# Performance work log

Hardware: AMD Instinct MI355X
Metric: run time of the kernel (lower is better)

## Reference

```python
import jax, jax.numpy as jnp
import numpy as np

N_NODES = 50000
N_EDGES = 800000
D_IN = 128
D_HID = 128


def setup_inputs() -> dict:
    key = jax.random.key(0)
    ks = jax.random.split(key, 9)
    x = jax.random.normal(ks[0], (N_NODES, D_IN), dtype=jnp.float32)
    edge_index = jax.random.randint(ks[1], (2, N_EDGES), 0, N_NODES, dtype=jnp.int64)
    s = 1.0 / np.sqrt(D_IN)
    # SAGEConv params: lin_l acts on mean-aggregated neighbors (has bias),
    # lin_r acts on the root/self features (no bias). Stored as [in, out].
    Wl1 = jax.random.uniform(ks[2], (D_IN, D_HID), jnp.float32, -s, s)
    Wr1 = jax.random.uniform(ks[3], (D_IN, D_HID), jnp.float32, -s, s)
    b1 = jax.random.uniform(ks[4], (D_HID,), jnp.float32, -s, s)
    Wl2 = jax.random.uniform(ks[5], (D_HID, D_HID), jnp.float32, -s, s)
    Wr2 = jax.random.uniform(ks[6], (D_HID, D_HID), jnp.float32, -s, s)
    b2 = jax.random.uniform(ks[7], (D_HID,), jnp.float32, -s, s)
    return {"x": x, "edge_index": edge_index, "Wl1": Wl1, "Wr1": Wr1,
            "b1": b1, "Wl2": Wl2, "Wr2": Wr2, "b2": b2}


def _sage_conv(h, src, dst, n_nodes, Wl, Wr, b):
    # gather neighbor features, mean-aggregate at targets (PyG mean aggr)
    msg = h[src]  # [E, d]
    summed = jax.ops.segment_sum(msg, dst, num_segments=n_nodes)  # [N, d]
    cnt = jax.ops.segment_sum(jnp.ones((src.shape[0], 1), h.dtype), dst,
                              num_segments=n_nodes)  # [N, 1]
    agg = summed / jnp.maximum(cnt, 1.0)  # isolated nodes -> 0, matches scatter-mean
    return agg @ Wl + b + h @ Wr


def reference(x, edge_index, Wl1, Wr1, b1, Wl2, Wr2, b2):
    src = edge_index[0]  # source nodes j (messages flow j -> i)
    dst = edge_index[1]  # target nodes i
    n = x.shape[0]
    h = _sage_conv(x, src, dst, n, Wl1, Wr1, b1)
    h = jax.nn.relu(h)  # dropout is identity in eval mode
    out = _sage_conv(h, src, dst, n, Wl2, Wr2, b2)
    return out
```

## Files before the change

### kernel.cpp

```cpp
#include <hip/hip_runtime.h>
#include <hip/hip_bf16.h>

#define DD 128
#define BSH 8
#define CHUNK 4096
#define MM_STREAMS 1024

typedef __attribute__((ext_vector_type(8))) short short8v;
typedef __attribute__((ext_vector_type(4))) float f32x4;

static __device__ __forceinline__ ushort f2bf(float f) {
    __hip_bfloat16 b = __float2bfloat16(f);
    return *reinterpret_cast<ushort*>(&b);
}


__global__ __launch_bounds__(256) void k_prep(const int* __restrict__ ei,
                                              int* __restrict__ hist, int E, int NB, int nblk,
                                              const float* __restrict__ x,
                                              ushort* __restrict__ xbf, int n4, int castBlocks,
                                              const float* __restrict__ Wl1,
                                              const float* __restrict__ Wr1,
                                              ushort* __restrict__ Wt1,
                                              const float* __restrict__ Wl2,
                                              const float* __restrict__ Wr2,
                                              ushort* __restrict__ Wt2) {
    __shared__ int lh[256];
    int t = threadIdx.x;
    int b = blockIdx.x;

    if (b < nblk) {
        lh[t] = 0;
        __syncthreads();
        int e0 = b * CHUNK;
        int e1 = min(e0 + CHUNK, E);
        for (int e = e0 + t; e < e1; e += 256)
            atomicAdd(&lh[ei[E + e] >> BSH], 1);
        __syncthreads();
        if (t < NB) hist[b * NB + t] = lh[t];
        return;
    }
    b -= nblk;
    if (b < castBlocks) {
        int i = b * 256 + t;
        if (i < n4) {
            float4 v = reinterpret_cast<const float4*>(x)[i];
            ushort4 o;
            o.x = f2bf(v.x); o.y = f2bf(v.y); o.z = f2bf(v.z); o.w = f2bf(v.w);
            reinterpret_cast<ushort4*>(xbf)[i] = o;
        }
        return;
    }
    b -= castBlocks;
    {
        const float* Wl = (b < 128) ? Wl1 : Wl2;
        const float* Wr = (b < 128) ? Wr1 : Wr2;
        ushort* Wt = (b < 128) ? Wt1 : Wt2;
        int idx = (b & 127) * 256 + t;
        int nn = idx >> 8, k = idx & 255;
        float v = (k < 128) ? Wl[k * 128 + nn] : Wr[(k - 128) * 128 + nn];
        Wt[nn * 256 + k] = f2bf(v);
    }
}

__global__ __launch_bounds__(1024) void k_hscan(int* __restrict__ hist,
                                                int* __restrict__ bbase,
                                                int nblk, int NB, int E) {
    __shared__ int part[4][256];
    __shared__ int s[256];
    int t = threadIdx.x;
    int b = t & 255, g = t >> 8;
    int q = (nblk + 3) >> 2;
    int lo = g * q, hi = min(lo + q, nblk);
    int sum = 0;
    if (b < NB)
        for (int blk = lo; blk < hi; ++blk) sum += hist[blk * NB + b];
    part[g][b] = sum;
    __syncthreads();
    if (g == 0) s[b] = part[0][b] + part[1][b] + part[2][b] + part[3][b];
    __syncthreads();
    for (int off = 1; off < 256; off <<= 1) {
        int v = 0;
        if (g == 0 && b >= off) v = s[b - off];
        __syncthreads();
        if (g == 0) s[b] += v;
        __syncthreads();
    }
    int base = (b == 0) ? 0 : s[b - 1];
    if (g == 0 && b < NB) bbase[b] = base;
    if (t == 0) bbase[NB] = E;
    int run = base;
    for (int gg = 0; gg < g; ++gg) run += part[gg][b];
    if (b < NB)
        for (int blk = lo; blk < hi; ++blk) {
            int tmp = hist[blk * NB + b];
            hist[blk * NB + b] = run;
            run += tmp;
        }
}

__global__ __launch_bounds__(256) void k_scatter(const int* __restrict__ ei,
                                                 const int* __restrict__ hist,
                                                 uint* __restrict__ pairs, int E, int NB) {
    __shared__ int lofs[256];
    __shared__ int lh[256];
    int t = threadIdx.x;
    int blk = blockIdx.x;
    lh[t] = 0;
    if (t < NB) lofs[t] = hist[blk * NB + t];
    __syncthreads();
    int e0 = blk * CHUNK, e1 = min(e0 + CHUNK, E);
    for (int e = e0 + t; e < e1; e += 256) {
        int sN = ei[e];
        int d = ei[E + e];
        int b = d >> BSH;
        int lp = atomicAdd(&lh[b], 1);
        pairs[lofs[b] + lp] = ((uint)(d & 255) << 16) | (uint)sN;
    }
}

__global__ __launch_bounds__(256) void k_csr(const uint* __restrict__ pairs,
                                             const int* __restrict__ bbase,
                                             int* __restrict__ rowptr,
                                             ushort* __restrict__ eidx,
                                             int n, int E, int NB) {
    __shared__ int lc[256];
    __shared__ int cur[256];
    int t = threadIdx.x;
    int b = blockIdx.x;
    int node0 = b << BSH;
    lc[t] = 0;
    __syncthreads();
    int r0 = bbase[b], r1 = bbase[b + 1];
    for (int i = r0 + t; i < r1; i += 256)
        atomicAdd(&lc[pairs[i] >> 16], 1);
    __syncthreads();
    int c0 = lc[t];
#pragma unroll
    for (int off = 1; off < 256; off <<= 1) {
        int u = (t >= off) ? lc[t - off] : 0;
        __syncthreads();
        lc[t] += u;
        __syncthreads();
    }
    int rp = r0 + lc[t] - c0;
    int node = node0 + t;
    if (node < n) rowptr[node] = rp;
    if (b == NB - 1 && t == 0) rowptr[n] = E;
    cur[t] = rp;
    __syncthreads();
    for (int i = r0 + t; i < r1; i += 256) {
        uint pr = pairs[i];
        int p = atomicAdd(&cur[pr >> 16], 1);
        eidx[p] = (ushort)(pr & 0xFFFFu);
    }
}


#define ACC8(v)                                    \
    acc[0] += __uint_as_float((v).x << 16);        \
    acc[1] += __uint_as_float((v).x & 0xffff0000u);\
    acc[2] += __uint_as_float((v).y << 16);        \
    acc[3] += __uint_as_float((v).y & 0xffff0000u);\
    acc[4] += __uint_as_float((v).z << 16);        \
    acc[5] += __uint_as_float((v).z & 0xffff0000u);\
    acc[6] += __uint_as_float((v).w << 16);        \
    acc[7] += __uint_as_float((v).w & 0xffff0000u);

__global__ __launch_bounds__(256) void k_aggb(const ushort* __restrict__ hin,
                                              const int* __restrict__ rowptr,
                                              const ushort* __restrict__ eidx,
                                              ushort* __restrict__ aggout, int n) {
    int wave = (int)((blockIdx.x * (unsigned)blockDim.x + threadIdx.x) >> 6);
    int lane = threadIdx.x & 63;
    int grp = lane >> 4;
    int c16 = lane & 15;
    int node = wave * 4 + grp;
    if (node >= n) return;

    int beg = rowptr[node], end = rowptr[node + 1];
    const uint4* base = reinterpret_cast<const uint4*>(hin);

    float acc[8];
#pragma unroll
    for (int i = 0; i < 8; ++i) acc[i] = 0.f;

    for (int e = beg; e < end; e += 4) {
        int m = end - e;
        int i0 = eidx[e];
        int i1 = eidx[e + (m > 1 ? 1 : 0)];
        int i2 = eidx[e + (m > 2 ? 2 : 0)];
        int i3 = eidx[e + (m > 3 ? 3 : 0)];
        uint4 v0 = base[(size_t)i0 * 16 + c16];
        uint4 v1 = base[(size_t)i1 * 16 + c16];
        uint4 v2 = base[(size_t)i2 * 16 + c16];
        uint4 v3 = base[(size_t)i3 * 16 + c16];
        ACC8(v0);
        if (m > 1) { ACC8(v1); }
        if (m > 2) { ACC8(v2); }
        if (m > 3) { ACC8(v3); }
    }

    float inv = 1.0f / fmaxf((float)(end - beg), 1.0f);
    uint4 o;
    o.x = ((uint)f2bf(acc[1] * inv) << 16) | (uint)f2bf(acc[0] * inv);
    o.y = ((uint)f2bf(acc[3] * inv) << 16) | (uint)f2bf(acc[2] * inv);
    o.z = ((uint)f2bf(acc[5] * inv) << 16) | (uint)f2bf(acc[4] * inv);
    o.w = ((uint)f2bf(acc[7] * inv) << 16) | (uint)f2bf(acc[6] * inv);
    reinterpret_cast<uint4*>(aggout)[(size_t)node * 16 + c16] = o;
}


__global__ __launch_bounds__(256, 8) void k_mm(const ushort* __restrict__ Alow,
                                               const ushort* __restrict__ Ahigh,
                                               const ushort* __restrict__ Wt,
                                               const float* __restrict__ bias,
                                               void* __restrict__ outp,
                                               int n, int ntiles, int relu, int outBf16) {
    int t = threadIdx.x;
    int wv = t >> 6;
    int l = t & 63;
    int lr = l & 15;
    int lk = l >> 4;
    int gw = blockIdx.x * 4 + wv;
    int nt = gw & 7;
    int stream = gw >> 3;

    short8v bf[8];
    const ushort* wbase = Wt + (size_t)(nt * 16 + lr) * 256 + lk * 8;
#pragma unroll
    for (int ks = 0; ks < 8; ++ks)
        bf[ks] = *reinterpret_cast<const short8v*>(wbase + ks * 32);

    int col = nt * 16 + lr;
    float bv = bias[col];

    for (int tile = stream; tile < ntiles; tile += MM_STREAMS) {
        int m0 = tile * 16;
        int arow = m0 + lr;
        if (arow >= n) arow = n - 1;
        const ushort* alo = Alow + (size_t)arow * DD + lk * 8;
        const ushort* ahi = Ahigh + (size_t)arow * DD + lk * 8;

        f32x4 acc = (f32x4){0.f, 0.f, 0.f, 0.f};
#pragma unroll
        for (int ks = 0; ks < 4; ++ks) {
            short8v af = *reinterpret_cast<const short8v*>(alo + ks * 32);
            acc = __builtin_amdgcn_mfma_f32_16x16x32_bf16(af, bf[ks], acc, 0, 0, 0);
        }
#pragma unroll
        for (int ks = 0; ks < 4; ++ks) {
            short8v af = *reinterpret_cast<const short8v*>(ahi + ks * 32);
            acc = __builtin_amdgcn_mfma_f32_16x16x32_bf16(af, bf[ks + 4], acc, 0, 0, 0);
        }

        int row0 = m0 + lk * 4;
#pragma unroll
        for (int r = 0; r < 4; ++r) {
            int row = row0 + r;
            if (row < n) {
                float v = acc[r] + bv;
                if (relu) v = fmaxf(v, 0.f);
                if (outBf16) {
                    reinterpret_cast<ushort*>(outp)[(size_t)row * DD + col] = f2bf(v);
                } else {
                    reinterpret_cast<float*>(outp)[(size_t)row * DD + col] = v;
                }
            }
        }
    }
}


extern "C" void kernel_launch(void* const* d_in, const int* in_sizes, int n_in,
                              void* d_out, int out_size, void* d_ws, size_t ws_size,
                              hipStream_t stream) {
    const float* x   = (const float*)d_in[0];
    const int*   ei  = (const int*)d_in[1];
    const float* Wl1 = (const float*)d_in[2];
    const float* Wr1 = (const float*)d_in[3];
    const float* b1  = (const float*)d_in[4];
    const float* Wl2 = (const float*)d_in[5];
    const float* Wr2 = (const float*)d_in[6];
    const float* b2  = (const float*)d_in[7];
    float* out = (float*)d_out;

    int n = in_sizes[0] / DD;
    int E = in_sizes[1] / 2;

    int NB   = (n + 255) >> 8;
    int nblk = (E + CHUNK - 1) / CHUNK;

    char* ws = (char*)d_ws;
    size_t off = 0;
    auto take = [&](size_t bytes) -> void* {
        void* p = ws + off;
        off = (off + bytes + 255) & ~(size_t)255;
        return p;
    };
    int* rowptr    = (int*)take(((size_t)n + 1) * 4);
    int* hist      = (int*)take((size_t)nblk * NB * 4);
    int* bbase     = (int*)take(((size_t)NB + 1) * 4);
    ushort* eidx   = (ushort*)take((size_t)E * 2 + 16);
    uint* pairs    = (uint*)take((size_t)E * 4);
    ushort* xbf    = (ushort*)take((size_t)n * DD * 2);
    ushort* hbf    = (ushort*)take((size_t)n * DD * 2);
    ushort* aggbf  = (ushort*)take((size_t)n * DD * 2);
    ushort* Wt1    = (ushort*)take((size_t)DD * 256 * 2);
    ushort* Wt2    = (ushort*)take((size_t)DD * 256 * 2);

    int ntiles = (n + 15) / 16;
    int n4 = n * DD / 4;
    int castBlocks = (n4 + 255) / 256;
    int prepBlocks = nblk + castBlocks + 256;

    k_prep<<<prepBlocks, 256, 0, stream>>>(ei, hist, E, NB, nblk,
                                           x, xbf, n4, castBlocks,
                                           Wl1, Wr1, Wt1, Wl2, Wr2, Wt2);
    k_hscan<<<1, 1024, 0, stream>>>(hist, bbase, nblk, NB, E);
    k_scatter<<<nblk, 256, 0, stream>>>(ei, hist, pairs, E, NB);
    k_csr<<<NB, 256, 0, stream>>>(pairs, bbase, rowptr, eidx, n, E, NB);

    int aggBlocks = (n + 15) / 16;
    int mmBlocks  = MM_STREAMS * 8 / 4;

    k_aggb<<<aggBlocks, 256, 0, stream>>>(xbf, rowptr, eidx, aggbf, n);
    k_mm<<<mmBlocks, 256, 0, stream>>>(aggbf, xbf, Wt1, b1, hbf, n, ntiles, 1, 1);
    k_aggb<<<aggBlocks, 256, 0, stream>>>(hbf, rowptr, eidx, aggbf, n);
    k_mm<<<mmBlocks, 256, 0, stream>>>(aggbf, hbf, Wt2, b2, out, n, ntiles, 0, 0);
}
```

Before: 182.5 us.

## Stage A tiles in swizzled LDS and share across all column waves

The matmul kernel is restructured so each 512-thread block loads a 32-row strip of the concatenated [agg|h] inputs into XOR-swizzled shared memory once. Its eight waves each handle one 16-column output slice from that shared tile. Before, eight separate waves re-read the same A rows from global memory in a persistent stream loop. The cost is reloading the weight fragments per block instead of per persistent wave, plus an LDS barrier, across about 1563 blocks.

Measured after the change: 159.9 us. -12.4%, faster.

```diff
diff --git a/kernel.cpp b/kernel.cpp
--- a/kernel.cpp
+++ b/kernel.cpp
@@ -4,7 +4,6 @@
 #define DD 128
 #define BSH 8
 #define CHUNK 4096
-#define MM_STREAMS 1024
 
 typedef __attribute__((ext_vector_type(8))) short short8v;
 typedef __attribute__((ext_vector_type(4))) float f32x4;
@@ -211,55 +210,62 @@
 }
 
 
-__global__ __launch_bounds__(256, 8) void k_mm(const ushort* __restrict__ Alow,
+__global__ __launch_bounds__(512, 8) void k_mm(const ushort* __restrict__ Alow,
                                                const ushort* __restrict__ Ahigh,
                                                const ushort* __restrict__ Wt,
                                                const float* __restrict__ bias,
                                                void* __restrict__ outp,
-                                               int n, int ntiles, int relu, int outBf16) {
-    int t = threadIdx.x;
+                                               int n, int relu, int outBf16) {
+    __shared__ ushort sA[32][256];
+
+    int t = threadIdx.x;
+    int row0 = blockIdx.x * 32;
+
+#pragma unroll
+    for (int i = t; i < 1024; i += 512) {
+        int r = i >> 5, c = i & 31;
+        int row = row0 + r;
+        if (row >= n) row = n - 1;
+        const ushort* src = (c < 16) ? (Alow + (size_t)row * DD + c * 8)
+                                     : (Ahigh + (size_t)row * DD + (c - 16) * 8);
+        uint4 v = *reinterpret_cast<const uint4*>(src);
+        int cs = (c & 16) | ((c ^ r) & 15);
+        *reinterpret_cast<uint4*>(&sA[r][cs * 8]) = v;
+    }
+    __syncthreads();
+
     int wv = t >> 6;
-    int l = t & 63;
-    int lr = l & 15;
-    int lk = l >> 4;
-    int gw = blockIdx.x * 4 + wv;
-    int nt = gw & 7;
-    int stream = gw >> 3;
+    int lane = t & 63;
+    int lr = lane & 15;
+    int lk = lane >> 4;
 
     short8v bf[8];
-    const ushort* wbase = Wt + (size_t)(nt * 16 + lr) * 256 + lk * 8;
+    const ushort* wbase = Wt + (size_t)(wv * 16 + lr) * 256 + lk * 8;
 #pragma unroll
     for (int ks = 0; ks < 8; ++ks)
         bf[ks] = *reinterpret_cast<const short8v*>(wbase + ks * 32);
 
-    int col = nt * 16 + lr;
+    int col = wv * 16 + lr;
     float bv = bias[col];
 
-    for (int tile = stream; tile < ntiles; tile += MM_STREAMS) {
-        int m0 = tile * 16;
-        int arow = m0 + lr;
-        if (arow >= n) arow = n - 1;
-        const ushort* alo = Alow + (size_t)arow * DD + lk * 8;
-        const ushort* ahi = Ahigh + (size_t)arow * DD + lk * 8;
-
+#pragma unroll
+    for (int sub = 0; sub < 2; ++sub) {
+        int m0 = sub * 16;
+        int r = m0 + lr;
         f32x4 acc = (f32x4){0.f, 0.f, 0.f, 0.f};
 #pragma unroll
-        for (int ks = 0; ks < 4; ++ks) {
-            short8v af = *reinterpret_cast<const short8v*>(alo + ks * 32);
+        for (int ks = 0; ks < 8; ++ks) {
+            int cc = ks * 4 + lk;
+            int cs = (cc & 16) | ((cc ^ r) & 15);
+            short8v af = *reinterpret_cast<const short8v*>(&sA[r][cs * 8]);
             acc = __builtin_amdgcn_mfma_f32_16x16x32_bf16(af, bf[ks], acc, 0, 0, 0);
         }
-#pragma unroll
-        for (int ks = 0; ks < 4; ++ks) {
-            short8v af = *reinterpret_cast<const short8v*>(ahi + ks * 32);
-            acc = __builtin_amdgcn_mfma_f32_16x16x32_bf16(af, bf[ks + 4], acc, 0, 0, 0);
-        }
-
-        int row0 = m0 + lk * 4;
-#pragma unroll
-        for (int r = 0; r < 4; ++r) {
-            int row = row0 + r;
+        int rowb = row0 + m0 + lk * 4;
+#pragma unroll
+        for (int q = 0; q < 4; ++q) {
+            int row = rowb + q;
             if (row < n) {
-                float v = acc[r] + bv;
+                float v = acc[q] + bv;
                 if (relu) v = fmaxf(v, 0.f);
                 if (outBf16) {
                     reinterpret_cast<ushort*>(outp)[(size_t)row * DD + col] = f2bf(v);
@@ -309,7 +315,6 @@
     ushort* Wt1    = (ushort*)take((size_t)DD * 256 * 2);
     ushort* Wt2    = (ushort*)take((size_t)DD * 256 * 2);
 
-    int ntiles = (n + 15) / 16;
     int n4 = n * DD / 4;
     int castBlocks = (n4 + 255) / 256;
     int prepBlocks = nblk + castBlocks + 256;
@@ -322,10 +327,10 @@
     k_csr<<<NB, 256, 0, stream>>>(pairs, bbase, rowptr, eidx, n, E, NB);
 
     int aggBlocks = (n + 15) / 16;
-    int mmBlocks  = MM_STREAMS * 8 / 4;
+    int mmBlocks  = (n + 31) / 32;
 
     k_aggb<<<aggBlocks, 256, 0, stream>>>(xbf, rowptr, eidx, aggbf, n);
-    k_mm<<<mmBlocks, 256, 0, stream>>>(aggbf, xbf, Wt1, b1, hbf, n, ntiles, 1, 1);
+    k_mm<<<mmBlocks, 512, 0, stream>>>(aggbf, xbf, Wt1, b1, hbf, n, 1, 1);
     k_aggb<<<aggBlocks, 256, 0, stream>>>(hbf, rowptr, eidx, aggbf, n);
-    k_mm<<<mmBlocks, 256, 0, stream>>>(aggbf, hbf, Wt2, b2, out, n, ntiles, 0, 0);
-}
+    k_mm<<<mmBlocks, 512, 0, stream>>>(aggbf, hbf, Wt2, b2, out, n, 0, 0);
+}
```
